# Optimization experiments

Measured on AMD Instinct MI355X. Metric: run time of the kernel, lower is better.

Reference implementation:

```python
import math
import jax, jax.numpy as jnp
import numpy as np

B = 2
N = 48           # max_atoms
A = 16           # num_atom_types
E = 5            # num_bond_types
HID = 384
NH = 8
HD = HID // NH   # 48
LYR = 4
MLP = 4 * HID
L = N + N * N    # 2352 sequence length (nodes + flattened edges)


def setup_inputs() -> dict:
    key = jax.random.key(0)
    ks = iter(jax.random.split(key, 48))
    r = lambda *s: jax.random.normal(next(ks), s, jnp.float32) * 0.02
    d = {
        "x": jax.random.normal(next(ks), (B, N, A), jnp.float32),
        "adj": jax.random.normal(next(ks), (B, N, N, E), jnp.float32),
        "t": jax.random.uniform(next(ks), (B,), jnp.float32),
        # embeddings
        "node_w": r(A, HID), "node_b": jnp.zeros((HID,), jnp.float32),
        "edge_w": r(E, HID), "edge_b": jnp.zeros((HID,), jnp.float32),
        "pos": r(L, HID),
        # timestep MLP (SinusoidalPositionalEmbedding(HID) -> Linear(HID,4H) -> SiLU -> Linear(4H,H))
        "t_w1": r(HID, 4 * HID), "t_b1": jnp.zeros((4 * HID,), jnp.float32),
        "t_w2": r(4 * HID, HID), "t_b2": jnp.zeros((HID,), jnp.float32),
        # stacked per-layer params
        "ada1_w": r(LYR, HID, 2 * HID), "ada1_b": jnp.zeros((LYR, 2 * HID), jnp.float32),
        "ada2_w": r(LYR, HID, 2 * HID), "ada2_b": jnp.zeros((LYR, 2 * HID), jnp.float32),
        "q_w": r(LYR, HID, HID), "q_b": jnp.zeros((LYR, HID), jnp.float32),
        "k_w": r(LYR, HID, HID), "k_b": jnp.zeros((LYR, HID), jnp.float32),
        "v_w": r(LYR, HID, HID), "v_b": jnp.zeros((LYR, HID), jnp.float32),
        "o_w": r(LYR, HID, HID), "o_b": jnp.zeros((LYR, HID), jnp.float32),
        "m1_w": r(LYR, HID, MLP), "m1_b": jnp.zeros((LYR, MLP), jnp.float32),
        "m2_w": r(LYR, MLP, HID), "m2_b": jnp.zeros((LYR, HID), jnp.float32),
        # final norm + heads (heads random instead of zero-init so output is informative)
        "fn_g": jnp.ones((HID,), jnp.float32), "fn_b": jnp.zeros((HID,), jnp.float32),
        "on_w": r(HID, A), "on_b": jnp.zeros((A,), jnp.float32),
        "oe_w": r(HID, E), "oe_b": jnp.zeros((E,), jnp.float32),
    }
    return d


def _ln(z):
    # LayerNorm(elementwise_affine=False), eps=1e-5
    mu = z.mean(-1, keepdims=True)
    var = z.var(-1, keepdims=True)
    return (z - mu) * jax.lax.rsqrt(var + 1e-5)


def _forward(x, adj, t, node_w, node_b, edge_w, edge_b, pos,
             t_w1, t_b1, t_w2, t_b2,
             ada1_w, ada1_b, ada2_w, ada2_b,
             q_w, q_b, k_w, k_b, v_w, v_b, o_w, o_b,
             m1_w, m1_b, m2_w, m2_b,
             fn_g, fn_b, on_w, on_b, oe_w, oe_b):
    b = x.shape[0]
    # embed nodes and edges, concat into sequence [b, L, HID]
    h_nodes = x @ node_w + node_b                       # [b, N, H]
    h_edges = adj.reshape(b, N * N, E) @ edge_w + edge_b  # [b, N*N, H]
    h = jnp.concatenate([h_nodes, h_edges], axis=1) + pos[None]
    # sinusoidal timestep embedding -> cond [b, HID]
    half = HID // 2
    freqs = jnp.exp(-math.log(10000.0) * jnp.arange(half, dtype=jnp.float32) / half)
    ang = t[:, None].astype(jnp.float32) * freqs[None, :]
    temb = jnp.concatenate([jnp.sin(ang), jnp.cos(ang)], axis=-1)
    cond = jax.nn.silu(temb @ t_w1 + t_b1) @ t_w2 + t_b2
    inv_scale = 1.0 / math.sqrt(HD)
    for i in range(LYR):
        # AdaLN 1 + attention
        sc, sh = jnp.split(cond @ ada1_w[i] + ada1_b[i], 2, axis=-1)
        n = _ln(h) * (1.0 + sc[:, None, :]) + sh[:, None, :]
        q = (n @ q_w[i] + q_b[i]).reshape(b, L, NH, HD)
        k = (n @ k_w[i] + k_b[i]).reshape(b, L, NH, HD)
        v = (n @ v_w[i] + v_b[i]).reshape(b, L, NH, HD)
        scores = jnp.einsum('bqhd,bkhd->bhqk', q, k) * inv_scale
        attn = jax.nn.softmax(scores, axis=-1)
        ao = jnp.einsum('bhqk,bkhd->bqhd', attn, v).reshape(b, L, HID)
        h = h + ao @ o_w[i] + o_b[i]
        # AdaLN 2 + MLP (exact GELU as in nn.GELU default)
        sc2, sh2 = jnp.split(cond @ ada2_w[i] + ada2_b[i], 2, axis=-1)
        n2 = _ln(h) * (1.0 + sc2[:, None, :]) + sh2[:, None, :]
        h = h + jax.nn.gelu(n2 @ m1_w[i] + m1_b[i], approximate=False) @ m2_w[i] + m2_b[i]
    h = _ln(h) * fn_g + fn_b
    node_out = h[:, :N] @ on_w + on_b                   # [b, N, A]
    edge_out = (h[:, N:] @ oe_w + oe_b).reshape(b, N, N, E)
    return node_out, edge_out


def reference(x, adj, t, node_w, node_b, edge_w, edge_b, pos,
              t_w1, t_b1, t_w2, t_b2,
              ada1_w, ada1_b, ada2_w, ada2_b,
              q_w, q_b, k_w, k_b, v_w, v_b, o_w, o_b,
              m1_w, m1_b, m2_w, m2_b,
              fn_g, fn_b, on_w, on_b, oe_w, oe_b):
    return _forward(x, adj, t, node_w, node_b, edge_w, edge_b, pos,
                    t_w1, t_b1, t_w2, t_b2,
                    ada1_w, ada1_b, ada2_w, ada2_b,
                    q_w, q_b, k_w, k_b, v_w, v_b, o_w, o_b,
                    m1_w, m1_b, m2_w, m2_b,
                    fn_g, fn_b, on_w, on_b, oe_w, oe_b)
```

## Files before the change

kernel.cpp:

```cpp
#include <hip/hip_runtime.h>
#include <hip/hip_bf16.h>
#include <math.h>

typedef __hip_bfloat16 bf16;
typedef __attribute__((ext_vector_type(8))) short short8;
typedef __attribute__((ext_vector_type(4))) float f32x4;

#define B_ 2
#define N_ 48
#define A_ 16
#define E_ 5
#define HID 384
#define NHD 8
#define HD 48
#define LYR 4
#define MLPD 1536
#define L_ 2352
#define M_ 4704
#define VLP 2432
#define QSCALE 0.20823513f

#define WQ_  0LL
#define WK_  589824LL
#define WV_  1179648LL
#define WO_  1769472LL
#define WM1_ 2359296LL
#define WM2_ 4718592LL
#define WTOT 7077888
#define BQ_  0
#define BK_  1536
#define BV_  3072
#define BO_  4608
#define BM1_ 6144
#define BM2_ 12288
#define BTOT 13824

static __device__ __forceinline__ float b2f(bf16 v) { return __bfloat162float(v); }
static __device__ __forceinline__ float us2f(unsigned short u) {
    return __uint_as_float(((unsigned)u) << 16);
}
static __device__ __forceinline__ unsigned short f2us(float f) {
    bf16 h = __float2bfloat16(f);
    return *reinterpret_cast<unsigned short*>(&h);
}
static __device__ __forceinline__ float ldv(const float* p, size_t i) { return p[i]; }
static __device__ __forceinline__ float ldv(const bf16*  p, size_t i) { return b2f(p[i]); }
static __device__ __forceinline__ void  stv(float* p, size_t i, float v) { p[i] = v; }
static __device__ __forceinline__ void  stv(bf16*  p, size_t i, float v) { p[i] = __float2bfloat16(v); }
static __device__ __forceinline__ float4 ld4(const float* p, size_t i) {
    return *reinterpret_cast<const float4*>(p + i);
}
static __device__ __forceinline__ float4 ld4(const bf16* p, size_t i) {
    ushort4 u = *reinterpret_cast<const ushort4*>(p + i);
    return make_float4(us2f(u.x), us2f(u.y), us2f(u.z), us2f(u.w));
}

__global__ void k_detect(const void* w, int* flag) {
    if (threadIdx.x == 0 && blockIdx.x == 0) {
        const bf16* p = (const bf16*)w;
        int isf = 0;
        for (int i = 0; i < 256; ++i) {
            float v = fabsf(b2f(p[i]));
            if (!(v <= 1000.0f)) { isf = 1; break; }
        }
        *flag = isf;
    }
}

template <typename T>
static __device__ void prepw_body(
    const T* q_w, const T* k_w, const T* v_w, const T* o_w,
    const T* m1_w, const T* m2_w, bf16* wbt)
{
    __shared__ unsigned short Ts[64][72];
    const int z = blockIdx.y;
    const int kind = z >> 2, l = z & 3;
    const T* src; int K, N; long long dbase;
    switch (kind) {
        case 0: src = q_w;  K = 384;  N = 384;  dbase = WQ_;  break;
        case 1: src = k_w;  K = 384;  N = 384;  dbase = WK_;  break;
        case 2: src = v_w;  K = 384;  N = 384;  dbase = WV_;  break;
        case 3: src = o_w;  K = 384;  N = 384;  dbase = WO_;  break;
        case 4: src = m1_w; K = 384;  N = 1536; dbase = WM1_; break;
        default: src = m2_w; K = 1536; N = 384; dbase = WM2_; break;
    }
    const int Nt = N >> 6;
    const int tiles = (K >> 6) * Nt;
    if (blockIdx.x >= tiles) return;
    const int tk = blockIdx.x / Nt, tn = blockIdx.x % Nt;
    const int k0 = tk*64, n0 = tn*64;
    const size_t soff = (size_t)l * K * N;
    const size_t doff = (size_t)dbase + (size_t)l * K * N;
    const int tid = threadIdx.x;
    {
        const int kk = tid >> 2, nc = (tid & 3) * 16;
        #pragma unroll
        for (int j = 0; j < 16; ++j)
            Ts[kk][nc + j] = f2us(ldv(src, soff + (size_t)(k0 + kk)*N + n0 + nc + j));
    }
    __syncthreads();
    {
        const int nn = tid >> 2, kc = (tid & 3) * 16;
        unsigned short tmp[16];
        #pragma unroll
        for (int j = 0; j < 16; ++j) tmp[j] = Ts[kc + j][nn];
        unsigned short* dst = (unsigned short*)wbt + doff + (size_t)(n0 + nn)*K + k0 + kc;
        *reinterpret_cast<short8*>(dst)     = *reinterpret_cast<short8*>(&tmp[0]);
        *reinterpret_cast<short8*>(dst + 8) = *reinterpret_cast<short8*>(&tmp[8]);
    }
}

__global__ __launch_bounds__(256) void k_prepw(
    const void* q_w, const void* k_w, const void* v_w, const void* o_w,
    const void* m1_w, const void* m2_w, const int* __restrict__ fl, bf16* __restrict__ wbt)
{
    if (*fl) prepw_body<float>((const float*)q_w, (const float*)k_w, (const float*)v_w,
                               (const float*)o_w, (const float*)m1_w, (const float*)m2_w, wbt);
    else     prepw_body<bf16>((const bf16*)q_w, (const bf16*)k_w, (const bf16*)v_w,
                              (const bf16*)o_w, (const bf16*)m1_w, (const bf16*)m2_w, wbt);
}

template <typename T>
static __device__ void prepb_body(
    const T* q_b, const T* k_b, const T* v_b, const T* o_b,
    const T* m1_b, const T* m2_b, bf16* bb)
{
    for (int i = threadIdx.x; i < BTOT; i += 256) {
        float v;
        if      (i < BK_)  v = ldv(q_b,  i);
        else if (i < BV_)  v = ldv(k_b,  i - BK_);
        else if (i < BO_)  v = ldv(v_b,  i - BV_);
        else if (i < BM1_) v = ldv(o_b,  i - BO_);
        else if (i < BM2_) v = ldv(m1_b, i - BM1_);
        else               v = ldv(m2_b, i - BM2_);
        bb[i] = __float2bfloat16(v);
    }
}

__global__ __launch_bounds__(256) void k_prepb(
    const void* q_b, const void* k_b, const void* v_b, const void* o_b,
    const void* m1_b, const void* m2_b, const int* __restrict__ fl, bf16* __restrict__ bb)
{
    if (*fl) prepb_body<float>((const float*)q_b, (const float*)k_b, (const float*)v_b,
                               (const float*)o_b, (const float*)m1_b, (const float*)m2_b, bb);
    else     prepb_body<bf16>((const bf16*)q_b, (const bf16*)k_b, (const bf16*)v_b,
                              (const bf16*)o_b, (const bf16*)m1_b, (const bf16*)m2_b, bb);
}

template <typename T>
static __device__ void embed_body(
    const T* x, const T* adj, const T* node_w, const T* node_b,
    const T* edge_w, const T* edge_b, const T* pos, float* h)
{
    const int bl = blockIdx.x;
    const int b = bl / L_, l = bl % L_;
    const int c = threadIdx.x;
    float acc;
    if (l < N_) {
        acc = ldv(node_b, c);
        const size_t xr = (size_t)(b*N_ + l)*A_;
        #pragma unroll
        for (int a = 0; a < A_; ++a) acc += ldv(x, xr + a) * ldv(node_w, (size_t)a*HID + c);
    } else {
        const int e = l - N_;
        acc = ldv(edge_b, c);
        const size_t ar = ((size_t)b*N_*N_ + e)*E_;
        #pragma unroll
        for (int j = 0; j < E_; ++j) acc += ldv(adj, ar + j) * ldv(edge_w, (size_t)j*HID + c);
    }
    h[(size_t)bl*HID + c] = acc + ldv(pos, (size_t)l*HID + c);
}

__global__ __launch_bounds__(384) void k_embed(
    const void* x, const void* adj, const void* node_w, const void* node_b,
    const void* edge_w, const void* edge_b, const void* pos,
    const int* __restrict__ fl, float* __restrict__ h)
{
    if (*fl) embed_body<float>((const float*)x, (const float*)adj, (const float*)node_w,
                               (const float*)node_b, (const float*)edge_w, (const float*)edge_b,
                               (const float*)pos, h);
    else     embed_body<bf16>((const bf16*)x, (const bf16*)adj, (const bf16*)node_w,
                              (const bf16*)node_b, (const bf16*)edge_w, (const bf16*)edge_b,
                              (const bf16*)pos, h);
}

template <typename T>
static __device__ void cond1_body(const T* t, const T* t_w1, const T* t_b1, float* hid)
{
    __shared__ float temb[HID];
    __shared__ float red[4][64];
    const int b = blockIdx.x, jb = blockIdx.y, tid = threadIdx.x;
    const float tv = ldv(t, b);
    for (int c = tid; c < HID; c += 256) {
        int i = (c < 192) ? c : c - 192;
        float f = expf(-9.2103403719761836f * (float)i / 192.0f);
        float ang = tv * f;
        temb[c] = (c < 192) ? sinf(ang) : cosf(ang);
    }
    __syncthreads();
    const int ko = tid >> 6, jo = tid & 63;
    const int j = jb*64 + jo;
    float acc = 0.f;
    for (int i = ko*96; i < (ko + 1)*96; ++i)
        acc += temb[i] * ldv(t_w1, (size_t)i*4*HID + j);
    red[ko][jo] = acc;
    __syncthreads();
    if (ko == 0) {
        float a = red[0][jo] + red[1][jo] + red[2][jo] + red[3][jo] + ldv(t_b1, j);
        hid[(size_t)b*4*HID + j] = a / (1.0f + expf(-a));
    }
}

__global__ __launch_bounds__(256) void k_cond1(
    const void* t, const void* t_w1, const void* t_b1,
    const int* __restrict__ fl, float* __restrict__ hid)
{
    if (*fl) cond1_body<float>((const float*)t, (const float*)t_w1, (const float*)t_b1, hid);
    else     cond1_body<bf16>((const bf16*)t, (const bf16*)t_w1, (const bf16*)t_b1, hid);
}

template <typename T>
static __device__ void cond2_body(const T* t_w2, const T* t_b2, const float* hid, float* part)
{
    __shared__ float hs[128];
    const int b = blockIdx.x, ch = blockIdx.y, c = threadIdx.x;
    const int j0 = ch*128;
    if (c < 128) hs[c] = hid[(size_t)b*4*HID + j0 + c];
    __syncthreads();
    float acc = (ch == 0) ? ldv(t_b2, c) : 0.f;
    for (int jj = 0; jj < 128; ++jj)
        acc += hs[jj] * ldv(t_w2, (size_t)(j0 + jj)*HID + c);
    part[((size_t)b*12 + ch)*HID + c] = acc;
}

__global__ __launch_bounds__(384) void k_cond2(
    const void* t_w2, const void* t_b2, const int* __restrict__ fl,
    const float* __restrict__ hid, float* __restrict__ part)
{
    if (*fl) cond2_body<float>((const float*)t_w2, (const float*)t_b2, hid, part);
    else     cond2_body<bf16>((const bf16*)t_w2, (const bf16*)t_b2, hid, part);
}

template <typename T>
static __device__ void cond3_body(
    const T* ada1_w, const T* ada1_b, const T* ada2_w, const T* ada2_b,
    const float* part, float* ada_out)
{
    __shared__ float cs[HID];
    const int slot = blockIdx.x / 3, ob = blockIdx.x % 3, b = blockIdx.y;
    const int tid = threadIdx.x;
    for (int c = tid; c < HID; c += 256) {
        float s = 0.f;
        #pragma unroll
        for (int ch = 0; ch < 12; ++ch) s += part[((size_t)b*12 + ch)*HID + c];
        cs[c] = s;
    }
    __syncthreads();
    const int layer = slot >> 1, which = slot & 1;
    const int o = ob*256 + tid;
    const T* W  = which ? ada2_w : ada1_w;
    const T* Bi = which ? ada2_b : ada1_b;
    float acc = ldv(Bi, (size_t)layer*768 + o);
    const size_t wb = (size_t)layer*HID*768 + o;
    for (int c = 0; c < HID; ++c) acc += cs[c] * ldv(W, wb + (size_t)c*768);
    ada_out[((size_t)slot*B_ + b)*768 + o] = acc;
}

__global__ __launch_bounds__(256) void k_cond3(
    const void* ada1_w, const void* ada1_b, const void* ada2_w, const void* ada2_b,
    const int* __restrict__ fl, const float* __restrict__ part, float* __restrict__ ada_out)
{
    if (*fl) cond3_body<float>((const float*)ada1_w, (const float*)ada1_b,
                               (const float*)ada2_w, (const float*)ada2_b, part, ada_out);
    else     cond3_body<bf16>((const bf16*)ada1_w, (const bf16*)ada1_b,
                              (const bf16*)ada2_w, (const bf16*)ada2_b, part, ada_out);
}

__global__ __launch_bounds__(256) void k_adaln(
    const float* __restrict__ h, const float* __restrict__ ada,
    bf16* __restrict__ n, int slot)
{
    const int row  = blockIdx.x * 4 + (threadIdx.x >> 6);
    const int lane = threadIdx.x & 63;
    const int b = row / L_;
    const float* hr = h + (size_t)row*HID;
    float v[6]; float s = 0.f, ss = 0.f;
    #pragma unroll
    for (int j = 0; j < 6; ++j) { float t = hr[lane + j*64]; v[j] = t; s += t; ss += t*t; }
    #pragma unroll
    for (int off = 32; off; off >>= 1) { s += __shfl_xor(s, off); ss += __shfl_xor(ss, off); }
    const float mu = s * (1.0f/HID);
    const float rs = rsqrtf(fmaxf(ss * (1.0f/HID) - mu*mu, 0.0f) + 1e-5f);
    const float* ap = ada + ((size_t)slot*B_ + b)*768;
    bf16* nr = n + (size_t)row*HID;
    #pragma unroll
    for (int j = 0; j < 6; ++j) {
        int c = lane + j*64;
        nr[c] = __float2bfloat16((v[j] - mu)*rs*(1.0f + ap[c]) + ap[384 + c]);
    }
}

static __device__ __forceinline__ void gemm_epilogue(
    f32x4 (&acc)[2][2], float bcol0, float bcol1,
    bf16* Cb, float* Cf, int M, int N, int act, int mode,
    int bm, int bn, int wm, int wn, int quad, int c)
{
    const float bcol[2] = {bcol0, bcol1};
    #pragma unroll
    for (int mi = 0; mi < 2; ++mi)
        #pragma unroll
        for (int ni = 0; ni < 2; ++ni) {
            const int col = bn + wn*32 + ni*16 + c;
            #pragma unroll
            for (int r = 0; r < 4; ++r) {
                const int row = bm + wm*32 + mi*16 + quad*4 + r;
                if (row < M) {
                    float v = acc[mi][ni][r] + bcol[ni];
                    if (act) v = 0.5f * v * (1.0f + erff(v * 0.70710678118654752f));
                    if (mode == 1) Cf[(size_t)row*N + col] += v;
                    else if (mode == 0) Cb[(size_t)row*N + col] = __float2bfloat16(v);
                    else if (mode == 3) Cb[(size_t)row*N + col] = __float2bfloat16(v * QSCALE);
                    else {
                        const int b   = row >= L_ ? 1 : 0;
                        const int key = row - b*L_;
                        const int hh  = col / 48, d = col - hh*48;
                        Cb[((size_t)(b*8 + hh)*48 + d)*VLP + key] = __float2bfloat16(v);
                    }
                }
            }
        }
}

template <typename T>
static __device__ void gemm_body(
    const bf16* A, const T* W, long long woff, const T* bias, long long boff,
    bf16* Cb, float* Cf, int M, int N, int K, int act, int mode)
{
    __shared__ __align__(16) unsigned short As[64][72];
    __shared__ __align__(16) unsigned short Bt[64][72];
    const int tid  = threadIdx.x;
    const int wv   = tid >> 6, lane = tid & 63;
    const int quad = lane >> 4, c = lane & 15;
    const int wm = wv & 1, wn = wv >> 1;
    const int bm = blockIdx.x * 64, bn = blockIdx.y * 64;
    const int arow = tid >> 3, ach = tid & 7;
    f32x4 acc[2][2] = {{{0.f,0.f,0.f,0.f},{0.f,0.f,0.f,0.f}},
                       {{0.f,0.f,0.f,0.f},{0.f,0.f,0.f,0.f}}};
    for (int k0 = 0; k0 < K; k0 += 64) {
        short8 av[2]; float4 w0[2], w1[2];
        #pragma unroll
        for (int i = 0; i < 2; ++i) {
            const int row = i*32 + arow;
            av[i] = short8{0,0,0,0,0,0,0,0};
            if (bm + row < M)
                av[i] = *reinterpret_cast<const short8*>(
                            A + (size_t)(bm + row)*K + k0 + ach*8);
            const size_t wrow = (size_t)woff + (size_t)(k0 + i*32 + arow)*N + bn + ach*8;
            w0[i] = ld4(W, wrow);
            w1[i] = ld4(W, wrow + 4);
        }
        __syncthreads();
        #pragma unroll
        for (int i = 0; i < 2; ++i) {
            *reinterpret_cast<short8*>(&As[i*32 + arow][ach*8]) = av[i];
            const int kk = i*32 + arow, nb0 = ach*8;
            Bt[nb0+0][kk] = f2us(w0[i].x); Bt[nb0+1][kk] = f2us(w0[i].y);
            Bt[nb0+2][kk] = f2us(w0[i].z); Bt[nb0+3][kk] = f2us(w0[i].w);
            Bt[nb0+4][kk] = f2us(w1[i].x); Bt[nb0+5][kk] = f2us(w1[i].y);
            Bt[nb0+6][kk] = f2us(w1[i].z); Bt[nb0+7][kk] = f2us(w1[i].w);
        }
        __syncthreads();
        #pragma unroll
        for (int ks = 0; ks < 2; ++ks) {
            short8 af[2], bfr[2];
            #pragma unroll
            for (int mi = 0; mi < 2; ++mi)
                af[mi] = *reinterpret_cast<const short8*>(
                             &As[wm*32 + mi*16 + c][ks*32 + quad*8]);
            #pragma unroll
            for (int ni = 0; ni < 2; ++ni)
                bfr[ni] = *reinterpret_cast<const short8*>(
                              &Bt[wn*32 + ni*16 + c][ks*32 + quad*8]);
            #pragma unroll
            for (int mi = 0; mi < 2; ++mi)
                #pragma unroll
                for (int ni = 0; ni < 2; ++ni)
                    acc[mi][ni] = __builtin_amdgcn_mfma_f32_16x16x32_bf16(
                                      af[mi], bfr[ni], acc[mi][ni], 0, 0, 0);
        }
    }
    gemm_epilogue(acc, ldv(bias, (size_t)boff + bn + wn*32 + c),
                  ldv(bias, (size_t)boff + bn + wn*32 + 16 + c),
                  Cb, Cf, M, N, act, mode, bm, bn, wm, wn, quad, c);
}

__global__ __launch_bounds__(256) void k_gemm(
    const bf16* __restrict__ A, const void* W, long long woff, const void* bias, long long boff,
    bf16* Cb, float* Cf, int M, int N, int K, int act, int mode,
    const int* __restrict__ fl)
{
    if (*fl) gemm_body<float>(A, (const float*)W, woff, (const float*)bias, boff,
                              Cb, Cf, M, N, K, act, mode);
    else     gemm_body<bf16>(A, (const bf16*)W, woff, (const bf16*)bias, boff,
                             Cb, Cf, M, N, K, act, mode);
}

__global__ __launch_bounds__(256) void k_gemm_qkv(
    const bf16* __restrict__ A,
    const void* qw, const void* kw, const void* vw,
    const void* qb, const void* kb, const void* vb,
    long long woff, long long boff,
    bf16* Cq, bf16* Ck, bf16* Cv, const int* __restrict__ fl)
{
    const int z = blockIdx.z;
    const void* W  = (z == 0) ? qw : (z == 1) ? kw : vw;
    const void* Bi = (z == 0) ? qb : (z == 1) ? kb : vb;
    bf16* C        = (z == 0) ? Cq : (z == 1) ? Ck : Cv;
    const int mode = (z == 0) ? 3 : (z == 2) ? 2 : 0;
    if (*fl) gemm_body<float>(A, (const float*)W, woff, (const float*)Bi, boff,
                              C, nullptr, M_, HID, HID, 0, mode);
    else     gemm_body<bf16>(A, (const bf16*)W, woff, (const bf16*)Bi, boff,
                             C, nullptr, M_, HID, HID, 0, mode);
}

static __device__ void gemm_t_body(
    const bf16* A, const bf16* Wt, long long woff, const bf16* bias, long long boff,
    bf16* Cb, float* Cf, int M, int N, int K, int act, int mode)
{
    __shared__ __align__(16) unsigned short As[64][72];
    __shared__ __align__(16) unsigned short Bt[64][72];
    const int tid  = threadIdx.x;
    const int wv   = tid >> 6, lane = tid & 63;
    const int quad = lane >> 4, c = lane & 15;
    const int wm = wv & 1, wn = wv >> 1;
    const int bm = blockIdx.x * 64, bn = blockIdx.y * 64;
    const int arow = tid >> 3, ach = tid & 7;
    f32x4 acc[2][2] = {{{0.f,0.f,0.f,0.f},{0.f,0.f,0.f,0.f}},
                       {{0.f,0.f,0.f,0.f},{0.f,0.f,0.f,0.f}}};
    for (int k0 = 0; k0 < K; k0 += 64) {
        short8 av[2], wv8[2];
        #pragma unroll
        for (int i = 0; i < 2; ++i) {
            const int row = i*32 + arow;
            av[i] = short8{0,0,0,0,0,0,0,0};
            if (bm + row < M)
                av[i] = *reinterpret_cast<const short8*>(
                            A + (size_t)(bm + row)*K + k0 + ach*8);
            wv8[i] = *reinterpret_cast<const short8*>(
                         Wt + (size_t)woff + (size_t)(bn + row)*K + k0 + ach*8);
        }
        __syncthreads();
        #pragma unroll
        for (int i = 0; i < 2; ++i) {
            *reinterpret_cast<short8*>(&As[i*32 + arow][ach*8]) = av[i];
            *reinterpret_cast<short8*>(&Bt[i*32 + arow][ach*8]) = wv8[i];
        }
        __syncthreads();
        #pragma unroll
        for (int ks = 0; ks < 2; ++ks) {
            short8 af[2], bfr[2];
            #pragma unroll
            for (int mi = 0; mi < 2; ++mi)
                af[mi] = *reinterpret_cast<const short8*>(
                             &As[wm*32 + mi*16 + c][ks*32 + quad*8]);
            #pragma unroll
            for (int ni = 0; ni < 2; ++ni)
                bfr[ni] = *reinterpret_cast<const short8*>(
                              &Bt[wn*32 + ni*16 + c][ks*32 + quad*8]);
            #pragma unroll
            for (int mi = 0; mi < 2; ++mi)
                #pragma unroll
                for (int ni = 0; ni < 2; ++ni)
                    acc[mi][ni] = __builtin_amdgcn_mfma_f32_16x16x32_bf16(
                                      af[mi], bfr[ni], acc[mi][ni], 0, 0, 0);
        }
    }
    gemm_epilogue(acc, b2f(bias[boff + bn + wn*32 + c]),
                  b2f(bias[boff + bn + wn*32 + 16 + c]),
                  Cb, Cf, M, N, act, mode, bm, bn, wm, wn, quad, c);
}

__global__ __launch_bounds__(256) void k_gemm_t(
    const bf16* __restrict__ A, const bf16* __restrict__ Wt, long long woff,
    const bf16* __restrict__ bias, long long boff,
    bf16* Cb, float* Cf, int M, int N, int K, int act, int mode)
{
    gemm_t_body(A, Wt, woff, bias, boff, Cb, Cf, M, N, K, act, mode);
}

__global__ __launch_bounds__(256) void k_gemm_qkv_t(
    const bf16* __restrict__ A, const bf16* __restrict__ wbt, const bf16* __restrict__ bb,
    int lyr, bf16* Cq, bf16* Ck, bf16* Cv)
{
    const int z = blockIdx.z;
    long long woff; long long boff; bf16* C; int mode;
    if (z == 0)      { woff = WQ_ + (long long)lyr*147456; boff = BQ_ + lyr*384; C = Cq; mode = 3; }
    else if (z == 1) { woff = WK_ + (long long)lyr*147456; boff = BK_ + lyr*384; C = Ck; mode = 0; }
    else             { woff = WV_ + (long long)lyr*147456; boff = BV_ + lyr*384; C = Cv; mode = 2; }
    gemm_t_body(A, wbt, woff, bb, boff, C, nullptr, M_, HID, HID, 0, mode);
}

__global__ __launch_bounds__(512) void k_attn(
    const bf16* __restrict__ q, const bf16* __restrict__ k,
    const bf16* __restrict__ vt, bf16* __restrict__ ao)
{
    __shared__ __align__(16) unsigned short Ks[2][64][80];
    __shared__ __align__(16) unsigned short Vt[2][48][72];
    __shared__ __align__(16) unsigned short Pq[8][16][72];
    const int tid  = threadIdx.x;
    const int w    = tid >> 6, lane = tid & 63;
    const int quad = lane >> 4, c = lane & 15;
    const int qt = w & 3, sp = w >> 2;
    const int bh = blockIdx.y;
    const size_t base  = (size_t)(bh >> 3)*L_*HID + (size_t)(bh & 7)*HD;
    const size_t vbase = (size_t)bh*48*VLP;
    const int q0 = blockIdx.x*64 + qt*16;
    const bool qvalid = q0 < L_;
    const int qrow = qvalid ? (q0 + c) : c;

    short8 qf0, qf1;
    {
        const unsigned short* qp = (const unsigned short*)(q + base + (size_t)qrow*HID);
        qf0 = *reinterpret_cast<const short8*>(qp + quad*8);
        if (quad < 2) qf1 = *reinterpret_cast<const short8*>(qp + 32 + quad*8);
        else          qf1 = short8{0,0,0,0,0,0,0,0};
    }
    f32x4 o0 = {0.f,0.f,0.f,0.f}, o1 = {0.f,0.f,0.f,0.f}, o2 = {0.f,0.f,0.f,0.f};
    float m = -3.0e38f, lsum = 0.f;

    const int t256 = tid & 255, grp = tid >> 8;
    const int krow0 = t256 >> 3, kch = t256 & 7;
    const int krow1 = 32 + krow0;
    const int vd0 = krow0;
    const int vd1 = 32 + (krow0 & 15);
    const bool vl1 = (t256 < 128);
    const unsigned short* kq = (const unsigned short*)(k + base);
    const unsigned short* vq = (const unsigned short*)(vt + vbase);
    const short8 Z8 = short8{0,0,0,0,0,0,0,0};
    short8 kr0 = Z8, kr1 = Z8, vr0, vr1 = Z8;
    {
        const int kb0 = grp*1216;
        if (kch < 6) {
            kr0 = *reinterpret_cast<const short8*>(kq + (size_t)(kb0 + krow0)*HID + kch*8);
            kr1 = *reinterpret_cast<const short8*>(kq + (size_t)(kb0 + krow1)*HID + kch*8);
        }
        vr0 = *reinterpret_cast<const short8*>(vq + (size_t)vd0*VLP + kb0 + kch*8);
        if (vl1) vr1 = *reinterpret_cast<const short8*>(vq + (size_t)vd1*VLP + kb0 + kch*8);
    }

    for (int tt = 0; tt < 19; ++tt) {
        __syncthreads();
        *reinterpret_cast<short8*>(&Ks[grp][krow0][kch*8]) = kr0;
        *reinterpret_cast<short8*>(&Ks[grp][krow1][kch*8]) = kr1;
        *reinterpret_cast<short8*>(&Vt[grp][vd0][kch*8])   = vr0;
        if (vl1) *reinterpret_cast<short8*>(&Vt[grp][vd1][kch*8]) = vr1;
        __syncthreads();
        if (tt < 18) {
            const int nb0 = grp*1216 + (tt + 1)*64;
            if (kch < 6) {
                kr0 = *reinterpret_cast<const short8*>(kq + (size_t)(nb0 + krow0)*HID + kch*8);
                kr1 = *reinterpret_cast<const short8*>(kq + (size_t)(nb0 + krow1)*HID + kch*8);
            }
            vr0 = *reinterpret_cast<const short8*>(vq + (size_t)vd0*VLP + nb0 + kch*8);
            if (vl1) vr1 = *reinterpret_cast<const short8*>(vq + (size_t)vd1*VLP + nb0 + kch*8);
        }

        const int kt = sp*1216 + tt*64;
        float sv[16];
        #pragma unroll
        for (int t = 0; t < 4; ++t) {
            f32x4 acc = {0.f,0.f,0.f,0.f};
            short8 a0 = *reinterpret_cast<const short8*>(&Ks[sp][t*16 + c][quad*8]);
            short8 a1 = *reinterpret_cast<const short8*>(&Ks[sp][t*16 + c][32 + quad*8]);
            acc = __builtin_amdgcn_mfma_f32_16x16x32_bf16(a0, qf0, acc, 0, 0, 0);
            acc = __builtin_amdgcn_mfma_f32_16x16x32_bf16(a1, qf1, acc, 0, 0, 0);
            #pragma unroll
            for (int r = 0; r < 4; ++r) sv[t*4 + r] = acc[r];
        }
        if (sp == 1 && tt >= 17) {
            #pragma unroll
            for (int t = 0; t < 4; ++t)
                #pragma unroll
                for (int r = 0; r < 4; ++r)
                    if (kt + t*16 + quad*4 + r >= L_) sv[t*4 + r] = -3.0e38f;
        }
        float tmax = sv[0];
        #pragma unroll
        for (int i = 1; i < 16; ++i) tmax = fmaxf(tmax, sv[i]);
        tmax = fmaxf(tmax, __shfl_xor(tmax, 16));
        tmax = fmaxf(tmax, __shfl_xor(tmax, 32));
        const float mn = fmaxf(m, tmax);
        const float alpha = exp2f(m - mn);
        m = mn;
        float psum = 0.f;
        unsigned short pv[16];
        #pragma unroll
        for (int i = 0; i < 16; ++i) {
            const float p = exp2f(sv[i] - m);
            psum += p;
            pv[i] = f2us(p);
        }
        lsum = lsum * alpha + psum;
        o0 *= alpha; o1 *= alpha; o2 *= alpha;
        #pragma unroll
        for (int t = 0; t < 4; ++t)
            *reinterpret_cast<ushort4*>(&Pq[w][c][t*16 + quad*4]) =
                make_ushort4(pv[t*4+0], pv[t*4+1], pv[t*4+2], pv[t*4+3]);
        #pragma unroll
        for (int s = 0; s < 2; ++s) {
            short8 pf  = *reinterpret_cast<const short8*>(&Pq[w][c][s*32 + quad*8]);
            short8 vf0 = *reinterpret_cast<const short8*>(&Vt[sp][c][s*32 + quad*8]);
            short8 vf1 = *reinterpret_cast<const short8*>(&Vt[sp][16 + c][s*32 + quad*8]);
            short8 vf2 = *reinterpret_cast<const short8*>(&Vt[sp][32 + c][s*32 + quad*8]);
            o0 = __builtin_amdgcn_mfma_f32_16x16x32_bf16(vf0, pf, o0, 0, 0, 0);
            o1 = __builtin_amdgcn_mfma_f32_16x16x32_bf16(vf1, pf, o1, 0, 0, 0);
            o2 = __builtin_amdgcn_mfma_f32_16x16x32_bf16(vf2, pf, o2, 0, 0, 0);
        }
    }
    float lw = lsum;
    lw += __shfl_xor(lw, 16);
    lw += __shfl_xor(lw, 32);
    float* Mg = (float*)&Ks[0][0][0];
    __syncthreads();
    if (sp == 1) {
        float* dst = Mg + (size_t)(qt*64 + lane)*14;
        dst[0] = o0[0]; dst[1] = o0[1]; dst[2]  = o0[2]; dst[3]  = o0[3];
        dst[4] = o1[0]; dst[5] = o1[1]; dst[6]  = o1[2]; dst[7]  = o1[3];
        dst[8] = o2[0]; dst[9] = o2[1]; dst[10] = o2[2]; dst[11] = o2[3];
        dst[12] = m; dst[13] = lw;
    }
    __syncthreads();
    if (sp == 0 && qvalid) {
        const float* src = Mg + (size_t)(qt*64 + lane)*14;
        const float m2 = src[12], l2 = src[13];
        const float mm = fmaxf(m, m2);
        const float a1 = exp2f(m - mm), a2 = exp2f(m2 - mm);
        const float inv = 1.0f / (lw*a1 + l2*a2);
        unsigned short* orow = (unsigned short*)(ao + base + (size_t)(q0 + c)*HID);
        const f32x4 ot[3] = {o0, o1, o2};
        #pragma unroll
        for (int dt = 0; dt < 3; ++dt) {
            ushort4 w4;
            w4.x = f2us((ot[dt][0]*a1 + src[dt*4+0]*a2) * inv);
            w4.y = f2us((ot[dt][1]*a1 + src[dt*4+1]*a2) * inv);
            w4.z = f2us((ot[dt][2]*a1 + src[dt*4+2]*a2) * inv);
            w4.w = f2us((ot[dt][3]*a1 + src[dt*4+3]*a2) * inv);
            *reinterpret_cast<ushort4*>(orow + dt*16 + quad*4) = w4;
        }
    }
}

template <typename T, typename TO>
static __device__ void final_body(
    const float* h, const T* fn_g, const T* fn_b,
    const T* on_w, const T* on_b, const T* oe_w, const T* oe_b, TO* out)
{
    __shared__ float hf[HID];
    const int row = blockIdx.x;
    const int b = row / L_, l = row % L_;
    const int lane = threadIdx.x;
    const float* hr = h + (size_t)row*HID;
    float v[6]; float s = 0.f, ss = 0.f;
    #pragma unroll
    for (int j = 0; j < 6; ++j) { float t = hr[lane + j*64]; v[j] = t; s += t; ss += t*t; }
    #pragma unroll
    for (int off = 32; off; off >>= 1) { s += __shfl_xor(s, off); ss += __shfl_xor(ss, off); }
    const float mu = s * (1.0f/HID);
    const float rs = rsqrtf(fmaxf(ss * (1.0f/HID) - mu*mu, 0.0f) + 1e-5f);
    #pragma unroll
    for (int j = 0; j < 6; ++j) {
        int c = lane + j*64;
        hf[c] = (v[j] - mu) * rs * ldv(fn_g, c) + ldv(fn_b, c);
    }
    __syncthreads();
    if (l < N_) {
        if (lane < A_) {
            float acc = ldv(on_b, lane);
            for (int c = 0; c < HID; ++c) acc += hf[c] * ldv(on_w, (size_t)c*A_ + lane);
            stv(out, (size_t)(b*N_ + l)*A_ + lane, acc);
        }
    } else {
        const int e = l - N_;
        if (lane < E_) {
            float acc = ldv(oe_b, lane);
            for (int c = 0; c < HID; ++c) acc += hf[c] * ldv(oe_w, (size_t)c*E_ + lane);
            stv(out, (size_t)B_*N_*A_ + ((size_t)b*N_*N_ + e)*E_ + lane, acc);
        }
    }
}

__global__ __launch_bounds__(64) void k_final(
    const float* __restrict__ h, const void* fn_g, const void* fn_b,
    const void* on_w, const void* on_b, const void* oe_w, const void* oe_b,
    const int* __restrict__ fl, void* out)
{
    if (*fl) final_body<float, float>(h, (const float*)fn_g, (const float*)fn_b,
                                      (const float*)on_w, (const float*)on_b,
                                      (const float*)oe_w, (const float*)oe_b, (float*)out);
    else     final_body<bf16, bf16>(h, (const bf16*)fn_g, (const bf16*)fn_b,
                                    (const bf16*)on_w, (const bf16*)on_b,
                                    (const bf16*)oe_w, (const bf16*)oe_b, (bf16*)out);
}

extern "C" void kernel_launch(void* const* d_in, const int* in_sizes, int n_in,
                              void* d_out, int out_size, void* d_ws, size_t ws_size,
                              hipStream_t stream) {
    const void* x      = d_in[0];
    const void* adj    = d_in[1];
    const void* t      = d_in[2];
    const void* node_w = d_in[3];
    const void* node_b = d_in[4];
    const void* edge_w = d_in[5];
    const void* edge_b = d_in[6];
    const void* pos    = d_in[7];
    const void* t_w1   = d_in[8];
    const void* t_b1   = d_in[9];
    const void* t_w2   = d_in[10];
    const void* t_b2   = d_in[11];
    const void* ada1_w = d_in[12];
    const void* ada1_b = d_in[13];
    const void* ada2_w = d_in[14];
    const void* ada2_b = d_in[15];
    const void* q_w    = d_in[16];
    const void* q_b    = d_in[17];
    const void* k_w    = d_in[18];
    const void* k_b    = d_in[19];
    const void* v_w    = d_in[20];
    const void* v_b    = d_in[21];
    const void* o_w    = d_in[22];
    const void* o_b    = d_in[23];
    const void* m1_w   = d_in[24];
    const void* m1_b   = d_in[25];
    const void* m2_w   = d_in[26];
    const void* m2_b   = d_in[27];
    const void* fn_g   = d_in[28];
    const void* fn_b   = d_in[29];
    const void* on_w   = d_in[30];
    const void* on_b   = d_in[31];
    const void* oe_w   = d_in[32];
    const void* oe_b   = d_in[33];

    const size_t SZ  = (size_t)M_ * HID;
    const size_t VTZ = (size_t)B_*NHD*HD*VLP;
    const size_t FLT = SZ + 12288 + (size_t)B_*4*HID + (size_t)B_*12*HID;
    const size_t M1FULL = (size_t)M_ * MLPD;
    const size_t BF_BASE = 3*SZ + VTZ;
    const size_t BF_BIG  = SZ + M1FULL;
    const size_t NEED      = 256 + sizeof(float)*FLT + sizeof(bf16)*BF_BASE;
    const size_t NEED_BIG  = 256 + sizeof(float)*FLT + sizeof(bf16)*BF_BIG;
    const size_t NEED_PREP = 256 + sizeof(float)*FLT
                           + sizeof(bf16)*(BF_BIG + WTOT + BTOT);
    if (ws_size < NEED) {
        hipMemsetAsync(d_out, 0, (size_t)out_size*sizeof(bf16), stream);
        return;
    }
    const bool big  = (ws_size >= NEED_BIG);
    const bool prep = (ws_size >= NEED_PREP);
    int*   fl   = (int*)d_ws;
    float* h    = (float*)((char*)d_ws + 256);
    float* ada  = h + SZ;
    float* hid  = ada + 12288;
    float* part = hid + (size_t)B_*4*HID;
    bf16* nb  = (bf16*)(part + (size_t)B_*12*HID);
    bf16* qb  = nb + SZ;
    bf16* kb  = qb + SZ;
    bf16* vtb = kb + SZ;
    bf16* m1c = kb;
    bf16* m1f = qb;
    bf16* wbt = nb + BF_BIG;
    bf16* bb  = wbt + WTOT;

    k_detect<<<1, 64, 0, stream>>>(node_w, fl);
    if (prep) {
        k_prepw<<<dim3(144, 24), 256, 0, stream>>>(q_w, k_w, v_w, o_w, m1_w, m2_w, fl, wbt);
        k_prepb<<<1, 256, 0, stream>>>(q_b, k_b, v_b, o_b, m1_b, m2_b, fl, bb);
    }
    k_embed<<<M_, HID, 0, stream>>>(x, adj, node_w, node_b, edge_w, edge_b, pos, fl, h);
    k_cond1<<<dim3(B_, 24), 256, 0, stream>>>(t, t_w1, t_b1, fl, hid);
    k_cond2<<<dim3(B_, 12), 384, 0, stream>>>(t_w2, t_b2, fl, hid, part);
    k_cond3<<<dim3(24, B_), 256, 0, stream>>>(ada1_w, ada1_b, ada2_w, ada2_b, fl, part, ada);
    for (int i = 0; i < LYR; ++i) {
        const long long woff   = (long long)i * HID * HID;
        const long long boff   = (long long)i * HID;
        const long long m1woff = (long long)i * HID * MLPD;
        const long long m1boff = (long long)i * MLPD;
        const long long m2woff = (long long)i * MLPD * HID;

        k_adaln<<<M_/4, 256, 0, stream>>>(h, ada, nb, 2*i);
        if (prep) {
            k_gemm_qkv_t<<<dim3(74, 6, 3), 256, 0, stream>>>(nb, wbt, bb, i, qb, kb, vtb);
            k_attn<<<dim3(37, B_*NHD), 512, 0, stream>>>(qb, kb, vtb, nb);
            k_gemm_t<<<dim3(74, 6), 256, 0, stream>>>(nb, wbt, WO_ + (long long)i*147456,
                                                      bb, BO_ + i*384,
                                                      nullptr, h, M_, HID, HID, 0, 1);
            k_adaln<<<M_/4, 256, 0, stream>>>(h, ada, nb, 2*i + 1);
            k_gemm_t<<<dim3(74, 24), 256, 0, stream>>>(nb, wbt, WM1_ + (long long)i*589824,
                                                       bb, BM1_ + i*MLPD,
                                                       m1f, nullptr, M_, MLPD, HID, 1, 0);
            k_gemm_t<<<dim3(74, 6), 256, 0, stream>>>(m1f, wbt, WM2_ + (long long)i*589824,
                                                      bb, BM2_ + i*384,
                                                      nullptr, h, M_, HID, MLPD, 0, 1);
        } else {
            k_gemm_qkv<<<dim3(74, 6, 3), 256, 0, stream>>>(nb, q_w, k_w, v_w, q_b, k_b, v_b,
                                                           woff, boff, qb, kb, vtb, fl);
            k_attn<<<dim3(37, B_*NHD), 512, 0, stream>>>(qb, kb, vtb, nb);
            k_gemm<<<dim3(74, 6), 256, 0, stream>>>(nb, o_w, woff, o_b, boff,
                                                    nullptr, h, M_, HID, HID, 0, 1, fl);
            k_adaln<<<M_/4, 256, 0, stream>>>(h, ada, nb, 2*i + 1);
            if (big) {
                k_gemm<<<dim3(74, 24), 256, 0, stream>>>(nb, m1_w, m1woff, m1_b, m1boff,
                                                         m1f, nullptr, M_, MLPD, HID, 1, 0, fl);
                k_gemm<<<dim3(74, 6), 256, 0, stream>>>(m1f, m2_w, m2woff, m2_b, boff,
                                                        nullptr, h, M_, HID, MLPD, 0, 1, fl);
            } else {
                for (int c = 0; c < 2; ++c) {
                    k_gemm<<<dim3(37, 24), 256, 0, stream>>>(nb + (size_t)c*2352*HID,
                                                             m1_w, m1woff, m1_b, m1boff,
                                                             m1c, nullptr, 2352, MLPD, HID, 1, 0, fl);
                    k_gemm<<<dim3(37, 6), 256, 0, stream>>>(m1c, m2_w, m2woff, m2_b, boff,
                                                            nullptr, h + (size_t)c*2352*HID,
                                                            2352, HID, MLPD, 0, 1, fl);
                }
            }
        }
    }
    k_final<<<M_, 64, 0, stream>>>(h, fn_g, fn_b, on_w, on_b, oe_w, oe_b, fl, (void*)d_out);
}
```

Before: 854.2 us.

## Double-buffer transposed GEMM via direct global-to-LDS loads; lazy softmax rescale

The transposed-weight GEMM now stages A and W tiles straight into LDS with global_load_lds into two buffers and an XOR-swizzled layout. The next K tile is fetched while MFMAs run on the current one, which cuts one sync per iteration and the register round trip. Out-of-range rows are clamped rather than zero-filled; they are presumably masked in the epilogue. In attention, the running-max rescale of the accumulators is skipped unless some lane's tile max exceeds the running max by more than 8 (log2 domain), and the max reduction is rewritten as a tree. Skipping the rescale leaves exponents up to 2^8 unnormalised in bf16 P, which is a small precision risk.

```diff
diff --git a/kernel.cpp b/kernel.cpp
--- a/kernel.cpp
+++ b/kernel.cpp
@@ -34,6 +34,10 @@
 #define BM1_ 6144
 #define BM2_ 12288
 #define BTOT 13824
+
+#define GLOAD16(gp, lp) __builtin_amdgcn_global_load_lds( \
+    (const __attribute__((address_space(1))) unsigned int*)(gp), \
+    (__attribute__((address_space(3))) unsigned int*)(lp), 16, 0, 0)
 
 static __device__ __forceinline__ float b2f(bf16 v) { return __bfloat162float(v); }
 static __device__ __forceinline__ float us2f(unsigned short u) {
@@ -427,46 +431,53 @@
     const bf16* A, const bf16* Wt, long long woff, const bf16* bias, long long boff,
     bf16* Cb, float* Cf, int M, int N, int K, int act, int mode)
 {
-    __shared__ __align__(16) unsigned short As[64][72];
-    __shared__ __align__(16) unsigned short Bt[64][72];
+    __shared__ __align__(16) unsigned short Tz[2][2][4096];
     const int tid  = threadIdx.x;
     const int wv   = tid >> 6, lane = tid & 63;
     const int quad = lane >> 4, c = lane & 15;
     const int wm = wv & 1, wn = wv >> 1;
     const int bm = blockIdx.x * 64, bn = blockIdx.y * 64;
-    const int arow = tid >> 3, ach = tid & 7;
+    const unsigned short* Ag = (const unsigned short*)A;
+    const unsigned short* Wg = (const unsigned short*)Wt + woff;
+    const int sr = tid >> 3;
+    const int csw0 = (((tid & 7) ^ (sr & 7)) << 3);
+    int ar0 = bm + sr;        ar0 = ar0 < M ? ar0 : M - 1;
+    int ar1 = bm + 32 + sr;   ar1 = ar1 < M ? ar1 : M - 1;
+    const int wr0 = bn + sr, wr1 = bn + 32 + sr;
+    const int ldso = tid * 8;
+
     f32x4 acc[2][2] = {{{0.f,0.f,0.f,0.f},{0.f,0.f,0.f,0.f}},
                        {{0.f,0.f,0.f,0.f},{0.f,0.f,0.f,0.f}}};
+
+    #define STAGE_T(buf, k0) do { \
+        GLOAD16(Ag + (size_t)ar0*K + (k0) + csw0, &Tz[buf][0][ldso]); \
+        GLOAD16(Ag + (size_t)ar1*K + (k0) + csw0, &Tz[buf][0][2048 + ldso]); \
+        GLOAD16(Wg + (size_t)wr0*K + (k0) + csw0, &Tz[buf][1][ldso]); \
+        GLOAD16(Wg + (size_t)wr1*K + (k0) + csw0, &Tz[buf][1][2048 + ldso]); \
+    } while (0)
+
+    STAGE_T(0, 0);
+    __syncthreads();
+    int cur = 0;
     for (int k0 = 0; k0 < K; k0 += 64) {
-        short8 av[2], wv8[2];
-        #pragma unroll
-        for (int i = 0; i < 2; ++i) {
-            const int row = i*32 + arow;
-            av[i] = short8{0,0,0,0,0,0,0,0};
-            if (bm + row < M)
-                av[i] = *reinterpret_cast<const short8*>(
-                            A + (size_t)(bm + row)*K + k0 + ach*8);
-            wv8[i] = *reinterpret_cast<const short8*>(
-                         Wt + (size_t)woff + (size_t)(bn + row)*K + k0 + ach*8);
-        }
-        __syncthreads();
-        #pragma unroll
-        for (int i = 0; i < 2; ++i) {
-            *reinterpret_cast<short8*>(&As[i*32 + arow][ach*8]) = av[i];
-            *reinterpret_cast<short8*>(&Bt[i*32 + arow][ach*8]) = wv8[i];
-        }
-        __syncthreads();
+        if (k0 + 64 < K) STAGE_T(cur ^ 1, k0 + 64);
         #pragma unroll
         for (int ks = 0; ks < 2; ++ks) {
             short8 af[2], bfr[2];
             #pragma unroll
-            for (int mi = 0; mi < 2; ++mi)
-                af[mi] = *reinterpret_cast<const short8*>(
-                             &As[wm*32 + mi*16 + c][ks*32 + quad*8]);
+            for (int mi = 0; mi < 2; ++mi) {
+                const int row = wm*32 + mi*16 + c;
+                const char* p = (const char*)&Tz[cur][0][0]
+                              + (row*128 + (((ks*64 + quad*16)) ^ ((row & 7) << 4)));
+                af[mi] = *reinterpret_cast<const short8*>(p);
+            }
             #pragma unroll
-            for (int ni = 0; ni < 2; ++ni)
-                bfr[ni] = *reinterpret_cast<const short8*>(
-                              &Bt[wn*32 + ni*16 + c][ks*32 + quad*8]);
+            for (int ni = 0; ni < 2; ++ni) {
+                const int row = wn*32 + ni*16 + c;
+                const char* p = (const char*)&Tz[cur][1][0]
+                              + (row*128 + (((ks*64 + quad*16)) ^ ((row & 7) << 4)));
+                bfr[ni] = *reinterpret_cast<const short8*>(p);
+            }
             #pragma unroll
             for (int mi = 0; mi < 2; ++mi)
                 #pragma unroll
@@ -474,7 +485,10 @@
                     acc[mi][ni] = __builtin_amdgcn_mfma_f32_16x16x32_bf16(
                                       af[mi], bfr[ni], acc[mi][ni], 0, 0, 0);
         }
-    }
+        __syncthreads();
+        cur ^= 1;
+    }
+    #undef STAGE_T
     gemm_epilogue(acc, b2f(bias[boff + bn + wn*32 + c]),
                   b2f(bias[boff + bn + wn*32 + 16 + c]),
                   Cb, Cf, M, N, act, mode, bm, bn, wm, wn, quad, c);
@@ -584,14 +598,20 @@
                 for (int r = 0; r < 4; ++r)
                     if (kt + t*16 + quad*4 + r >= L_) sv[t*4 + r] = -3.0e38f;
         }
-        float tmax = sv[0];
-        #pragma unroll
-        for (int i = 1; i < 16; ++i) tmax = fmaxf(tmax, sv[i]);
+        float tmax = fmaxf(fmaxf(fmaxf(sv[0], sv[1]),  fmaxf(sv[2],  sv[3])),
+                           fmaxf(fmaxf(sv[4], sv[5]),  fmaxf(sv[6],  sv[7])));
+        float tmx2 = fmaxf(fmaxf(fmaxf(sv[8], sv[9]),  fmaxf(sv[10], sv[11])),
+                           fmaxf(fmaxf(sv[12], sv[13]), fmaxf(sv[14], sv[15])));
+        tmax = fmaxf(tmax, tmx2);
         tmax = fmaxf(tmax, __shfl_xor(tmax, 16));
         tmax = fmaxf(tmax, __shfl_xor(tmax, 32));
-        const float mn = fmaxf(m, tmax);
-        const float alpha = exp2f(m - mn);
-        m = mn;
+        if (!__all(tmax <= m + 8.0f)) {
+            const float mn = fmaxf(m, tmax);
+            const float alpha = exp2f(m - mn);
+            m = mn;
+            lsum *= alpha;
+            o0 *= alpha; o1 *= alpha; o2 *= alpha;
+        }
         float psum = 0.f;
         unsigned short pv[16];
         #pragma unroll
@@ -600,8 +620,7 @@
             psum += p;
             pv[i] = f2us(p);
         }
-        lsum = lsum * alpha + psum;
-        o0 *= alpha; o1 *= alpha; o2 *= alpha;
+        lsum += psum;
         #pragma unroll
         for (int t = 0; t < 4; ++t)
             *reinterpret_cast<ushort4*>(&Pq[w][c][t*16 + quad*4]) =
```

Measured after the change: 818.1 us. 1.04x faster.
